# Performance work log

Measured on AMD Instinct MI355X. Metric: run time of the kernel, lower is better.

Reference implementation:

```python
import jax, jax.numpy as jnp
import numpy as np

N, D = 8192, 128

def _rbf_kernel(x, y):
    # InfoVAE-style kernel: exp(-mean((x_i - y_j)^2) / dim) = exp(-sqdist / dim^2)
    dim = x.shape[1]
    x2 = jnp.sum(x * x, axis=1)              # [n]
    y2 = jnp.sum(y * y, axis=1)              # [m]
    sqdist = x2[:, None] + y2[None, :] - 2.0 * (x @ y.T)  # [n, m]
    return jnp.exp(-sqdist / (dim * dim))


def setup_inputs() -> dict:
    key = jax.random.key(0)
    k1, k2 = jax.random.split(key)
    inputs = jax.random.normal(k1, (N, D), dtype=jnp.float32)
    true_samples = jax.random.normal(k2, (N, D), dtype=jnp.float32)
    return {"inputs": inputs, "true_samples": true_samples}


def reference(inputs, true_samples):
    x = true_samples  # samples from standard normal prior
    y = inputs
    k_xx = _rbf_kernel(x, x)
    k_yy = _rbf_kernel(y, y)
    k_xy = _rbf_kernel(x, y)
    mmd = jnp.mean(k_xx) + jnp.mean(k_yy) - 2.0 * jnp.mean(k_xy)
    return mmd
```

## Files before the change

### kernel.cpp

```cpp
#include <hip/hip_runtime.h>
#include <hip/hip_bf16.h>
#include <math.h>


#define NN 8192
#define DD 128
#define TZ 16384
#define TILES 64
#define NBLOCKS (TILES * (TILES + 1) / 2)

typedef __attribute__((ext_vector_type(8))) short bf16x8;
typedef __attribute__((ext_vector_type(4))) float f32x4;
typedef __attribute__((ext_vector_type(2))) float f32x2;

#if __has_builtin(__builtin_amdgcn_exp2f)
#define EXP2F __builtin_amdgcn_exp2f
#else
#define EXP2F exp2f
#endif

constexpr float LOG2E = 0x1.715476p+0f;
constexpr float S2 = LOG2E / 8192.0f;

constexpr size_t PLANE = 1048576;

constexpr size_t WS_NORM = 2048;
constexpr size_t WS_Z    = WS_NORM + (size_t)TZ * sizeof(float);

__device__ __forceinline__ void gload_lds16(const void* g, void* l) {
  __builtin_amdgcn_global_load_lds(
      (const __attribute__((address_space(1))) void*)g,
      (__attribute__((address_space(3))) void*)l, 16, 0, 0);
}

__global__ __launch_bounds__(256) void prep(
    const float* __restrict__ X, const float* __restrict__ Y,
    char* __restrict__ Zs, float* __restrict__ normZ,
    double* __restrict__ sums) {
  if (blockIdx.x == 0) sums[threadIdx.x] = 0.0;

  const int row = blockIdx.x * 4 + (threadIdx.x >> 6);
  const int lane = threadIdx.x & 63;
  const float* __restrict__ src =
      (row < NN) ? (X + (size_t)row * DD) : (Y + (size_t)(row - NN) * DD);
  const float2 v = *reinterpret_cast<const float2*>(src + 2 * lane);

  float n = v.x * v.x + v.y * v.y;

  const int ks = lane >> 4;
  const int quadc = (lane >> 2) & 3;
  const int inner = (lane & 3) * 4;
  char* dst = Zs + (size_t)ks * PLANE + (size_t)row * 64 +
              ((quadc ^ ((row >> 1) & 3)) << 4) + inner;
  *reinterpret_cast<__hip_bfloat162*>(dst) =
      __hip_bfloat162{__float2bfloat16(v.x), __float2bfloat16(v.y)};

#pragma unroll
  for (int o = 32; o > 0; o >>= 1) n += __shfl_down(n, o);
  if (lane == 0) normZ[row] = n * (-LOG2E / 16384.0f);
}

__device__ __forceinline__ int tri_start(int i) {
  return i * TILES - (i * (i - 1)) / 2;
}

__global__ __launch_bounds__(1024, 1) void mmd_mfma(
    const char* __restrict__ Zs, const float* __restrict__ normZ,
    double* __restrict__ sums) {
  __shared__ alignas(16) char lds[2 * 32768 + 256];

  const int t = blockIdx.x;
  int I = (int)((129.0 - sqrt(129.0 * 129.0 - 8.0 * (double)t)) * 0.5);
  if (I > 63) I = 63;
  if (I < 0) I = 0;
  while (I < 63 && tri_start(I + 1) <= t) ++I;
  while (I > 0 && tri_start(I) > t) --I;
  const int J = I + (t - tri_start(I));

  const int tid = threadIdx.x;
  const int lane = tid & 63, wave = tid >> 6;
  const int wr = wave >> 2, wc = wave & 3;
  const int lr = lane & 15, quad = lane >> 4;

  const char* srcA = Zs + (size_t)I * 16384 + wave * 1024 + (lane << 4);
  const char* srcB = Zs + (size_t)J * 16384 + wave * 1024 + (lane << 4);
  char* ldwA = lds + wave * 1024;
  char* ldwB = lds + 16384 + wave * 1024;

#define STAGE(s, buf) do {                                               \
    gload_lds16(srcA + (size_t)(s) * PLANE, ldwA + (buf) * 32768);       \
    gload_lds16(srcB + (size_t)(s) * PLANE, ldwB + (buf) * 32768);       \
  } while (0)

  const int csw = (quad ^ ((lr >> 1) & 3)) << 4;
  const char* aRd = lds + (wr * 64 + lr) * 64 + csw;
  const char* bRd = lds + 16384 + (wc * 64 + lr) * 64 + csw;

  bf16x8 a[4], b[4];
  f32x4 acc[4][4] = {};

#define LOADFRAGS(buf) do {                                              \
    _Pragma("unroll")                                                    \
    for (int i = 0; i < 4; ++i)                                          \
      a[i] = *reinterpret_cast<const bf16x8*>(aRd + (buf) * 32768 + i * 1024); \
    _Pragma("unroll")                                                    \
    for (int j = 0; j < 4; ++j)                                          \
      b[j] = *reinterpret_cast<const bf16x8*>(bRd + (buf) * 32768 + j * 1024); \
  } while (0)

#define MFMAS() do {                                                     \
    _Pragma("unroll")                                                    \
    for (int i = 0; i < 4; ++i)                                          \
      _Pragma("unroll")                                                  \
      for (int j = 0; j < 4; ++j)                                        \
        acc[i][j] = __builtin_amdgcn_mfma_f32_16x16x32_bf16(             \
            a[i], b[j], acc[i][j], 0, 0, 0);                             \
  } while (0)

  STAGE(0, 0);
  STAGE(1, 1);

  asm volatile("s_waitcnt vmcnt(2)\n\ts_barrier" ::: "memory");
  LOADFRAGS(0);
  asm volatile("s_waitcnt lgkmcnt(0)\n\ts_barrier" ::: "memory");
  __builtin_amdgcn_sched_barrier(0);
  STAGE(2, 0);
  __builtin_amdgcn_sched_barrier(0);
  MFMAS();

  asm volatile("s_waitcnt vmcnt(2)\n\ts_barrier" ::: "memory");
  LOADFRAGS(1);
  asm volatile("s_waitcnt lgkmcnt(0)\n\ts_barrier" ::: "memory");
  __builtin_amdgcn_sched_barrier(0);
  STAGE(3, 1);
  __builtin_amdgcn_sched_barrier(0);
  MFMAS();

  asm volatile("s_waitcnt vmcnt(2)\n\ts_barrier" ::: "memory");
  LOADFRAGS(0);
  asm volatile("s_waitcnt lgkmcnt(0)" ::: "memory");
  __builtin_amdgcn_sched_barrier(0);
  MFMAS();

  asm volatile("s_waitcnt vmcnt(0)\n\ts_barrier" ::: "memory");
  LOADFRAGS(1);
  asm volatile("s_waitcnt lgkmcnt(0)" ::: "memory");
  __builtin_amdgcn_sched_barrier(0);
  MFMAS();

#undef STAGE
#undef LOADFRAGS
#undef MFMAS

  const float* nzA = normZ + I * 256 + wr * 64;
  const float* nzB = normZ + J * 256 + wc * 64;
  f32x4 ar[4];
  float cb[4];
#pragma unroll
  for (int i = 0; i < 4; ++i)
    ar[i] = *reinterpret_cast<const f32x4*>(nzA + i * 16 + quad * 4);
#pragma unroll
  for (int j = 0; j < 4; ++j) cb[j] = nzB[j * 16 + lr];

  const f32x2 s2v = {S2, S2};
  f32x2 part01 = {0.f, 0.f}, part23 = {0.f, 0.f};
#pragma unroll
  for (int i = 0; i < 4; ++i) {
    const f32x2 ar01 = {ar[i].x, ar[i].y};
    const f32x2 ar23 = {ar[i].z, ar[i].w};
#pragma unroll
    for (int j = 0; j < 4; ++j) {
      const f32x2 rb2 = {cb[j], cb[j]};
      const f32x2 base01 = ar01 + rb2;
      const f32x2 base23 = ar23 + rb2;
      const f32x2 acc01 = {acc[i][j][0], acc[i][j][1]};
      const f32x2 acc23 = {acc[i][j][2], acc[i][j][3]};
      const f32x2 arg01 = __builtin_elementwise_fma(acc01, s2v, base01);
      const f32x2 arg23 = __builtin_elementwise_fma(acc23, s2v, base23);
      part01 += (f32x2){EXP2F(arg01.x), EXP2F(arg01.y)};
      part23 += (f32x2){EXP2F(arg23.x), EXP2F(arg23.y)};
    }
  }
  const f32x2 ps = part01 + part23;
  double local = (double)(ps.x + ps.y);
  double w = ((I < 32) == (J < 32)) ? 1.0 : -1.0;
  if (I != J) w += w;
  local *= w;

#pragma unroll
  for (int o = 32; o > 0; o >>= 1) local += __shfl_down(local, o);
  if (lane == 0)
    atomicAdd(&sums[((t & 15) << 4) | wave], local);
}

__global__ void finish(const double* __restrict__ s, float* __restrict__ out) {
  double v = s[threadIdx.x] + s[threadIdx.x + 64] + s[threadIdx.x + 128] +
             s[threadIdx.x + 192];
#pragma unroll
  for (int o = 32; o > 0; o >>= 1) v += __shfl_down(v, o);
  if (threadIdx.x == 0)
    out[0] = (float)(v * (1.0 / ((double)NN * (double)NN)));
}

extern "C" void kernel_launch(void* const* d_in, const int* in_sizes, int n_in,
                              void* d_out, int out_size, void* d_ws, size_t ws_size,
                              hipStream_t stream) {
  const float* y_inputs = (const float*)d_in[0];
  const float* x_true   = (const float*)d_in[1];
  float* out = (float*)d_out;

  char* ws = (char*)d_ws;
  double* sums = (double*)ws;
  float* normZ = (float*)(ws + WS_NORM);
  char* Zs = ws + WS_Z;

  prep<<<TZ / 4, 256, 0, stream>>>(x_true, y_inputs, Zs, normZ, sums);
  mmd_mfma<<<NBLOCKS, 1024, 0, stream>>>(Zs, normZ, sums);
  finish<<<1, 64, 0, stream>>>(sums, out);
}
```

Measured before the change: 119.1 us.

## Switch to persistent row-strip blocks reusing A tile across multiple B tiles

Replaces the one-block-per-256x256-triangle-tile launch with 768 blocks of 256 threads. Each block keeps a 128-row A strip resident in LDS and walks every SPLIT-th B tile along its row, double-buffering B loads across iterations and prefetching B norms into LDS. It also adds setprio around the MFMA bursts and reduces per-block partials through LDS before a single atomic. The aim is to cut repeated A loads and per-block launch and epilogue overhead, and to allow 3 blocks per CU. In exchange, work per block is uneven along the triangle and some blocks exit immediately.

```diff
diff --git a/kernel.cpp b/kernel.cpp
--- a/kernel.cpp
+++ b/kernel.cpp
@@ -6,8 +6,8 @@
 #define NN 8192
 #define DD 128
 #define TZ 16384
-#define TILES 64
-#define NBLOCKS (TILES * (TILES + 1) / 2)
+#define SPLIT 6
+#define NBLK (128 * SPLIT)
 
 typedef __attribute__((ext_vector_type(8))) short bf16x8;
 typedef __attribute__((ext_vector_type(4))) float f32x4;
@@ -23,6 +23,10 @@
 constexpr float S2 = LOG2E / 8192.0f;
 
 constexpr size_t PLANE = 1048576;
+
+#define LDS_B 32768
+#define LDS_NORM 49152
+#define LDS_RED 50176
 
 constexpr size_t WS_NORM = 2048;
 constexpr size_t WS_Z    = WS_NORM + (size_t)TZ * sizeof(float);
@@ -60,137 +64,163 @@
   if (lane == 0) normZ[row] = n * (-LOG2E / 16384.0f);
 }
 
-__device__ __forceinline__ int tri_start(int i) {
-  return i * TILES - (i * (i - 1)) / 2;
-}
-
-__global__ __launch_bounds__(1024, 1) void mmd_mfma(
+__global__ __launch_bounds__(256, 3) void mmd_mfma(
     const char* __restrict__ Zs, const float* __restrict__ normZ,
     double* __restrict__ sums) {
-  __shared__ alignas(16) char lds[2 * 32768 + 256];
-
-  const int t = blockIdx.x;
-  int I = (int)((129.0 - sqrt(129.0 * 129.0 - 8.0 * (double)t)) * 0.5);
-  if (I > 63) I = 63;
-  if (I < 0) I = 0;
-  while (I < 63 && tri_start(I + 1) <= t) ++I;
-  while (I > 0 && tri_start(I) > t) --I;
-  const int J = I + (t - tri_start(I));
+  __shared__ alignas(16) char lds[50176 + 64];
+
+  const int bid = blockIdx.x;
+  const int I = bid / SPLIT, s6 = bid % SPLIT;
+  const int rem = 127 - I - s6;
+  if (rem < 0) return;
+  const int nIter = rem / SPLIT + 1;
 
   const int tid = threadIdx.x;
   const int lane = tid & 63, wave = tid >> 6;
-  const int wr = wave >> 2, wc = wave & 3;
+  const int wr = wave >> 1, wc = wave & 1;
   const int lr = lane & 15, quad = lane >> 4;
 
-  const char* srcA = Zs + (size_t)I * 16384 + wave * 1024 + (lane << 4);
-  const char* srcB = Zs + (size_t)J * 16384 + wave * 1024 + (lane << 4);
-  char* ldwA = lds + wave * 1024;
-  char* ldwB = lds + 16384 + wave * 1024;
-
-#define STAGE(s, buf) do {                                               \
-    gload_lds16(srcA + (size_t)(s) * PLANE, ldwA + (buf) * 32768);       \
-    gload_lds16(srcB + (size_t)(s) * PLANE, ldwB + (buf) * 32768);       \
+  const float* nzA = normZ + I * 128 + wr * 64;
+  f32x4 ar[4];
+#pragma unroll
+  for (int i = 0; i < 4; ++i)
+    ar[i] = *reinterpret_cast<const f32x4*>(nzA + i * 16 + quad * 4);
+
+  const char* srcA0 = Zs + (size_t)(I * 128 + wave * 32) * 64 + lane * 16;
+  char* ldwA = lds + wave * 2048;
+#pragma unroll
+  for (int ks = 0; ks < 4; ++ks) {
+    gload_lds16(srcA0 + (size_t)ks * PLANE,        ldwA + ks * 8192);
+    gload_lds16(srcA0 + (size_t)ks * PLANE + 1024, ldwA + ks * 8192 + 1024);
+  }
+
+  int J = I + s6;
+  const char* srcB = Zs + (size_t)(J * 128 + wave * 32) * 64 + lane * 16;
+  const char* normB = (const char*)normZ + (size_t)J * 512 + lane * 16;
+
+#define STAGE_B(base, s, buf) do {                                          \
+    gload_lds16((base) + (size_t)(s) * PLANE,                               \
+                lds + LDS_B + (buf) * 8192 + wave * 2048);                  \
+    gload_lds16((base) + (size_t)(s) * PLANE + 1024,                        \
+                lds + LDS_B + (buf) * 8192 + wave * 2048 + 1024);           \
   } while (0)
+
+  STAGE_B(srcB, 0, 0);
+  STAGE_B(srcB, 1, 1);
+  asm volatile("s_waitcnt vmcnt(0)\n\ts_barrier" ::: "memory");
 
   const int csw = (quad ^ ((lr >> 1) & 3)) << 4;
   const char* aRd = lds + (wr * 64 + lr) * 64 + csw;
-  const char* bRd = lds + 16384 + (wc * 64 + lr) * 64 + csw;
+  const char* bRd = lds + LDS_B + (wc * 64 + lr) * 64 + csw;
 
   bf16x8 a[4], b[4];
-  f32x4 acc[4][4] = {};
-
-#define LOADFRAGS(buf) do {                                              \
-    _Pragma("unroll")                                                    \
-    for (int i = 0; i < 4; ++i)                                          \
-      a[i] = *reinterpret_cast<const bf16x8*>(aRd + (buf) * 32768 + i * 1024); \
-    _Pragma("unroll")                                                    \
-    for (int j = 0; j < 4; ++j)                                          \
-      b[j] = *reinterpret_cast<const bf16x8*>(bRd + (buf) * 32768 + j * 1024); \
+
+#define LOADFRAGS(ks, buf) do {                                             \
+    _Pragma("unroll")                                                       \
+    for (int i = 0; i < 4; ++i)                                             \
+      a[i] = *reinterpret_cast<const bf16x8*>(aRd + (ks) * 8192 + i * 1024);\
+    _Pragma("unroll")                                                       \
+    for (int j = 0; j < 4; ++j)                                             \
+      b[j] = *reinterpret_cast<const bf16x8*>(bRd + (buf) * 8192 + j * 1024);\
   } while (0)
 
-#define MFMAS() do {                                                     \
-    _Pragma("unroll")                                                    \
-    for (int i = 0; i < 4; ++i)                                          \
-      _Pragma("unroll")                                                  \
-      for (int j = 0; j < 4; ++j)                                        \
-        acc[i][j] = __builtin_amdgcn_mfma_f32_16x16x32_bf16(             \
-            a[i], b[j], acc[i][j], 0, 0, 0);                             \
+#define MFMAS() do {                                                        \
+    __builtin_amdgcn_s_setprio(1);                                          \
+    _Pragma("unroll")                                                       \
+    for (int i = 0; i < 4; ++i)                                             \
+      _Pragma("unroll")                                                     \
+      for (int j = 0; j < 4; ++j)                                           \
+        acc[i][j] = __builtin_amdgcn_mfma_f32_16x16x32_bf16(                \
+            a[i], b[j], acc[i][j], 0, 0, 0);                                \
+    __builtin_amdgcn_s_setprio(0);                                          \
   } while (0)
 
-  STAGE(0, 0);
-  STAGE(1, 1);
-
-  asm volatile("s_waitcnt vmcnt(2)\n\ts_barrier" ::: "memory");
-  LOADFRAGS(0);
-  asm volatile("s_waitcnt lgkmcnt(0)\n\ts_barrier" ::: "memory");
-  __builtin_amdgcn_sched_barrier(0);
-  STAGE(2, 0);
-  __builtin_amdgcn_sched_barrier(0);
-  MFMAS();
-
-  asm volatile("s_waitcnt vmcnt(2)\n\ts_barrier" ::: "memory");
-  LOADFRAGS(1);
-  asm volatile("s_waitcnt lgkmcnt(0)\n\ts_barrier" ::: "memory");
-  __builtin_amdgcn_sched_barrier(0);
-  STAGE(3, 1);
-  __builtin_amdgcn_sched_barrier(0);
-  MFMAS();
-
-  asm volatile("s_waitcnt vmcnt(2)\n\ts_barrier" ::: "memory");
-  LOADFRAGS(0);
-  asm volatile("s_waitcnt lgkmcnt(0)" ::: "memory");
-  __builtin_amdgcn_sched_barrier(0);
-  MFMAS();
-
-  asm volatile("s_waitcnt vmcnt(0)\n\ts_barrier" ::: "memory");
-  LOADFRAGS(1);
-  asm volatile("s_waitcnt lgkmcnt(0)" ::: "memory");
-  __builtin_amdgcn_sched_barrier(0);
-  MFMAS();
-
-#undef STAGE
+  const f32x2 s2v = {S2, S2};
+  double blockAcc = 0.0;
+
+  for (int it = 0; it < nIter; ++it) {
+    const char* srcBn = (it + 1 < nIter) ? srcB + SPLIT * 8192 : srcB;
+    f32x4 acc[4][4] = {};
+
+    asm volatile("s_waitcnt vmcnt(2)\n\ts_barrier" ::: "memory");
+    LOADFRAGS(0, 0);
+    asm volatile("s_waitcnt lgkmcnt(0)\n\ts_barrier" ::: "memory");
+    __builtin_amdgcn_sched_barrier(0);
+    STAGE_B(srcB, 2, 0);
+    gload_lds16(normB, lds + LDS_NORM);
+    __builtin_amdgcn_sched_barrier(0);
+    MFMAS();
+
+    asm volatile("s_waitcnt vmcnt(3)\n\ts_barrier" ::: "memory");
+    LOADFRAGS(1, 1);
+    asm volatile("s_waitcnt lgkmcnt(0)\n\ts_barrier" ::: "memory");
+    __builtin_amdgcn_sched_barrier(0);
+    STAGE_B(srcB, 3, 1);
+    __builtin_amdgcn_sched_barrier(0);
+    MFMAS();
+
+    asm volatile("s_waitcnt vmcnt(3)\n\ts_barrier" ::: "memory");
+    LOADFRAGS(2, 0);
+    asm volatile("s_waitcnt lgkmcnt(0)\n\ts_barrier" ::: "memory");
+    __builtin_amdgcn_sched_barrier(0);
+    STAGE_B(srcBn, 0, 0);
+    __builtin_amdgcn_sched_barrier(0);
+    MFMAS();
+
+    asm volatile("s_waitcnt vmcnt(2)\n\ts_barrier" ::: "memory");
+    LOADFRAGS(3, 1);
+    asm volatile("s_waitcnt lgkmcnt(0)\n\ts_barrier" ::: "memory");
+    __builtin_amdgcn_sched_barrier(0);
+    STAGE_B(srcBn, 1, 1);
+    __builtin_amdgcn_sched_barrier(0);
+    MFMAS();
+
+    float cb[4];
+#pragma unroll
+    for (int j = 0; j < 4; ++j)
+      cb[j] = *reinterpret_cast<const float*>(
+          lds + LDS_NORM + (wc * 64 + j * 16 + lr) * 4);
+
+    f32x2 part01 = {0.f, 0.f}, part23 = {0.f, 0.f};
+#pragma unroll
+    for (int i = 0; i < 4; ++i) {
+      const f32x2 ar01 = {ar[i].x, ar[i].y};
+      const f32x2 ar23 = {ar[i].z, ar[i].w};
+#pragma unroll
+      for (int j = 0; j < 4; ++j) {
+        const f32x2 rb2 = {cb[j], cb[j]};
+        const f32x2 base01 = ar01 + rb2;
+        const f32x2 base23 = ar23 + rb2;
+        const f32x2 acc01 = {acc[i][j][0], acc[i][j][1]};
+        const f32x2 acc23 = {acc[i][j][2], acc[i][j][3]};
+        const f32x2 arg01 = __builtin_elementwise_fma(acc01, s2v, base01);
+        const f32x2 arg23 = __builtin_elementwise_fma(acc23, s2v, base23);
+        part01 += (f32x2){EXP2F(arg01.x), EXP2F(arg01.y)};
+        part23 += (f32x2){EXP2F(arg23.x), EXP2F(arg23.y)};
+      }
+    }
+    const f32x2 ps = part01 + part23;
+    double w = ((I < 64) == (J < 64)) ? 1.0 : -1.0;
+    if (I != J) w += w;
+    blockAcc += (double)(ps.x + ps.y) * w;
+
+    J += SPLIT;
+    srcB += SPLIT * 8192;
+    normB += SPLIT * 512;
+  }
+
+#undef STAGE_B
 #undef LOADFRAGS
 #undef MFMAS
 
-  const float* nzA = normZ + I * 256 + wr * 64;
-  const float* nzB = normZ + J * 256 + wc * 64;
-  f32x4 ar[4];
-  float cb[4];
-#pragma unroll
-  for (int i = 0; i < 4; ++i)
-    ar[i] = *reinterpret_cast<const f32x4*>(nzA + i * 16 + quad * 4);
-#pragma unroll
-  for (int j = 0; j < 4; ++j) cb[j] = nzB[j * 16 + lr];
-
-  const f32x2 s2v = {S2, S2};
-  f32x2 part01 = {0.f, 0.f}, part23 = {0.f, 0.f};
-#pragma unroll
-  for (int i = 0; i < 4; ++i) {
-    const f32x2 ar01 = {ar[i].x, ar[i].y};
-    const f32x2 ar23 = {ar[i].z, ar[i].w};
-#pragma unroll
-    for (int j = 0; j < 4; ++j) {
-      const f32x2 rb2 = {cb[j], cb[j]};
-      const f32x2 base01 = ar01 + rb2;
-      const f32x2 base23 = ar23 + rb2;
-      const f32x2 acc01 = {acc[i][j][0], acc[i][j][1]};
-      const f32x2 acc23 = {acc[i][j][2], acc[i][j][3]};
-      const f32x2 arg01 = __builtin_elementwise_fma(acc01, s2v, base01);
-      const f32x2 arg23 = __builtin_elementwise_fma(acc23, s2v, base23);
-      part01 += (f32x2){EXP2F(arg01.x), EXP2F(arg01.y)};
-      part23 += (f32x2){EXP2F(arg23.x), EXP2F(arg23.y)};
-    }
-  }
-  const f32x2 ps = part01 + part23;
-  double local = (double)(ps.x + ps.y);
-  double w = ((I < 32) == (J < 32)) ? 1.0 : -1.0;
-  if (I != J) w += w;
-  local *= w;
-
-#pragma unroll
-  for (int o = 32; o > 0; o >>= 1) local += __shfl_down(local, o);
-  if (lane == 0)
-    atomicAdd(&sums[((t & 15) << 4) | wave], local);
+  asm volatile("s_waitcnt vmcnt(0)" ::: "memory");
+#pragma unroll
+  for (int o = 32; o > 0; o >>= 1) blockAcc += __shfl_down(blockAcc, o);
+  double* red = reinterpret_cast<double*>(lds + LDS_RED);
+  if (lane == 0) red[wave] = blockAcc;
+  __syncthreads();
+  if (tid == 0)
+    atomicAdd(&sums[bid & 255], red[0] + red[1] + red[2] + red[3]);
 }
 
 __global__ void finish(const double* __restrict__ s, float* __restrict__ out) {
@@ -215,6 +245,6 @@
   char* Zs = ws + WS_Z;
 
   prep<<<TZ / 4, 256, 0, stream>>>(x_true, y_inputs, Zs, normZ, sums);
-  mmd_mfma<<<NBLOCKS, 1024, 0, stream>>>(Zs, normZ, sums);
+  mmd_mfma<<<NBLK, 256, 0, stream>>>(Zs, normZ, sums);
   finish<<<1, 64, 0, stream>>>(sums, out);
 }
```

Measured after the change: 108.4 us. -8.9%, faster.
